# Kernel optimization log

Measured on AMD Instinct MI355X. Metric: run time of the kernel, lower is better.

## Reference

```python
import jax, jax.numpy as jnp
import numpy as np

B, N = 8, 48
NEMBED, EMBED_DIM, HID_DIM = 1000, 32, 32
IN_DIM = EMBED_DIM + 1  # feature dim after concatenating xfeat
N_OPS = 8  # exchangeable 3-tensor basis: identity + means over each nonempty axis subset


def setup_inputs() -> dict:
    key = jax.random.key(0)
    k1, k2, k3, k4, k5 = jax.random.split(key, 5)
    xcat = jax.random.randint(k1, (B, N), 0, NEMBED)
    xfeat = jax.random.normal(k2, (B, N), dtype=jnp.float32)
    embed_table = jax.random.normal(k3, (NEMBED, EMBED_DIM), dtype=jnp.float32)
    # SetEq3to3 coefficients: (in_dim, n_basis_ops, out_dim), Glorot-ish scale
    coefs = jax.random.normal(k4, (IN_DIM, N_OPS, HID_DIM), dtype=jnp.float32) * np.sqrt(2.0 / (IN_DIM + HID_DIM))
    eq_bias = jnp.zeros((HID_DIM,), dtype=jnp.float32)
    out_w = jax.random.normal(k5, (HID_DIM, 1), dtype=jnp.float32) * np.sqrt(1.0 / HID_DIM)
    out_b = jnp.zeros((1,), dtype=jnp.float32)
    return {"xcat": xcat, "xfeat": xfeat, "embed_table": embed_table,
            "coefs": coefs, "eq_bias": eq_bias, "out_w": out_w, "out_b": out_b}


def _set_eq3to3(t, coefs, eq_bias):
    # t: (B, d, n, n, n); coefs: (d, 8, h). Each basis op is a mean over a
    # subset of the three set axes (kept as size-1 dims so broadcasting restores shape).
    def mix(op, s):
        return jnp.einsum('bd...,dh->bh...', op, coefs[:, s, :])
    m_i = t.mean(axis=2, keepdims=True)
    m_j = t.mean(axis=3, keepdims=True)
    m_k = t.mean(axis=4, keepdims=True)
    m_ij = m_i.mean(axis=3, keepdims=True)
    m_ik = m_i.mean(axis=4, keepdims=True)
    m_jk = m_j.mean(axis=4, keepdims=True)
    m_ijk = m_ij.mean(axis=4, keepdims=True)
    out = (mix(t, 0) + mix(m_i, 1) + mix(m_j, 2) + mix(m_k, 3)
           + mix(m_ij, 4) + mix(m_ik, 5) + mix(m_jk, 6) + mix(m_ijk, 7))
    return out + eq_bias.reshape(1, -1, 1, 1, 1)  # (B, h, n, n, n)


def reference(xcat, xfeat, embed_table, coefs, eq_bias, out_w, out_b):
    e = embed_table[xcat]                                   # (B, n, d_e)
    x = jnp.concatenate([e, xfeat[..., None]], axis=-1)      # (B, n, d) with d = d_e + 1
    t = jnp.einsum('bid,bjd,bkd->bdijk', x, x, x)            # (B, d, n, n, n)
    y = _set_eq3to3(t, coefs, eq_bias)                       # (B, h, n, n, n)
    y = jnp.transpose(y, (0, 2, 3, 4, 1))                    # (B, n, n, n, h)
    y = jax.nn.relu(y)
    y = y.mean(axis=(1, 2, 3))                               # (B, h) mean pool
    y = jax.nn.relu(y)
    # dropout is inactive in eval mode (training=False)
    return y @ out_w + out_b                                 # (B, 1)
```

## Files before the change

### kernel.cpp

```cpp
#include <hip/hip_runtime.h>
#include <cstdint>
#include <cstddef>

#define BB 8
#define NN 48
#define DD 33
#define XS 40
#define KP 128
#define HH 32
#define MM (NN*NN)
#define NC (NN*HH)
#define TILE 96
#define TM (MM/TILE)
#define TN (NC/TILE)
#define SPLITM 4
#define MQ (TM/SPLITM)
#define NBLK (TN*SPLITM*BB)
#define LDK 136

typedef __attribute__((ext_vector_type(8))) _Float16 f16x8;
typedef __attribute__((ext_vector_type(4))) float f32x4;

__global__ void k_setup(const int* __restrict__ xcat, const float* __restrict__ xfeat,
                        const float* __restrict__ embed, const float* __restrict__ coefs,
                        float* __restrict__ xw, float* __restrict__ sw,
                        float* __restrict__ ct, float* __restrict__ hacc_g,
                        unsigned int* __restrict__ counter) {
    int b = blockIdx.x, t = threadIdx.x;
    if (b < BB) {
        for (int idx = t; idx < NN * XS; idx += 256) {
            int i = idx / XS, d = idx - i * XS;
            float v = 0.f;
            if (d < 32)       v = embed[xcat[b * NN + i] * 32 + d];
            else if (d == 32) v = xfeat[b * NN + i];
            xw[b * NN * XS + idx] = v;
        }
        __syncthreads();
        if (t < XS) {
            float a = 0.f;
            for (int i = 0; i < NN; ++i) a += xw[b * NN * XS + i * XS + t];
            sw[b * XS + t] = a * (1.0f / 48.0f);
        }
    } else if (b == BB) {
        for (int idx = t; idx < 8 * HH * XS; idx += 256) {
            int qh = idx / XS, d = idx - qh * XS;
            int q = qh >> 5, h = qh & 31;
            ct[idx] = (d < DD) ? coefs[(d * 8 + q) * HH + h] : 0.f;
        }
    } else {
        if (t < BB * HH) hacc_g[t] = 0.f;
        if (t == 0) *counter = 0u;
    }
}

__global__ __launch_bounds__(256, 2) void k_gemm(
        const float* __restrict__ xw, const float* __restrict__ sw,
        const float* __restrict__ ct, const float* __restrict__ eq_bias,
        float* __restrict__ hacc_g, unsigned int* __restrict__ counter,
        const float* __restrict__ out_w, const float* __restrict__ out_b,
        float* __restrict__ out) {
    __shared__ __align__(16) _Float16 As[TILE][LDK];
    __shared__ __align__(16) _Float16 Bs[TILE][LDK];
    __shared__ float gbuf[TILE];
    __shared__ float hacc[HH];
    __shared__ int lastFlag;

    int t = threadIdx.x;
    int bx = blockIdx.x, my = blockIdx.y, b = blockIdx.z;
    int N0 = bx * TILE;
    const float* xb = xw + b * NN * XS;
    const float* sb = sw + b * XS;

    if (t < HH) hacc[t] = 0.f;
    if (t < TILE) {
        int n = N0 + t, k = n >> 5, h = n & 31;
        const float* xk = xb + k * XS;
        const float* c4 = ct + (4 * HH + h) * XS;
        const float* c7 = ct + (7 * HH + h) * XS;
        float g = 0.f;
        for (int d = 0; d < DD; ++d) {
            float sd = sb[d];
            g += sd * sd * (c4[d] * xk[d] + c7[d] * sd);
        }
        gbuf[t] = g + eq_bias[h];
    }
    __syncthreads();

    for (int c = 0; c < 6; ++c) {
        int ch = c * 256 + t;
        int row = ch >> 4, d0 = (ch & 15) * 8;
        int n = N0 + row, k = n >> 5, h = n & 31;
        const float* xk = xb + k * XS;
        f16x8 v;
        if (d0 < 120) {
            int seg = (d0 >= 80) ? 2 : (d0 >= 40) ? 1 : 0;
            int d = d0 - seg * 40;
            const int QA[3] = {0, 2, 1}, QB[3] = {3, 6, 5};
            const float* ca = ct + (QA[seg] * HH + h) * XS + d;
            const float* cb = ct + (QB[seg] * HH + h) * XS + d;
            f32x4 ca0 = *(const f32x4*)(ca),     ca1 = *(const f32x4*)(ca + 4);
            f32x4 cb0 = *(const f32x4*)(cb),     cb1 = *(const f32x4*)(cb + 4);
            f32x4 xk0 = *(const f32x4*)(xk + d), xk1 = *(const f32x4*)(xk + d + 4);
            f32x4 sb0 = *(const f32x4*)(sb + d), sb1 = *(const f32x4*)(sb + d + 4);
            f32x4 r0 = ca0 * xk0 + cb0 * sb0;
            f32x4 r1 = ca1 * xk1 + cb1 * sb1;
            for (int e = 0; e < 4; ++e) { v[e] = (_Float16)r0[e]; v[4 + e] = (_Float16)r1[e]; }
        } else {
            v = (f16x8){0, 0, 0, 0, 0, 0, 0, 0};
            v[0] = (_Float16)gbuf[row];
        }
        *(f16x8*)&Bs[row][d0] = v;
    }

    auto buildA = [&](int mt) {
        int M0 = (my * MQ + mt) * TILE;
        for (int c = 0; c < 6; ++c) {
            int ch = c * 256 + t;
            int row = ch >> 4, d0 = (ch & 15) * 8;
            int grow = M0 + row;
            int i = grow / NN, j = grow - i * NN;
            f16x8 v;
            if (d0 < 120) {
                int seg = (d0 >= 80) ? 2 : (d0 >= 40) ? 1 : 0;
                int d = d0 - seg * 40;
                const float* p1 = (seg == 2) ? (xb + j * XS) : (xb + i * XS);
                const float* p2 = (seg == 0) ? (xb + j * XS) : sb;
                f32x4 a0 = *(const f32x4*)(p1 + d), a1 = *(const f32x4*)(p1 + d + 4);
                f32x4 b0 = *(const f32x4*)(p2 + d), b1 = *(const f32x4*)(p2 + d + 4);
                f32x4 r0 = a0 * b0, r1 = a1 * b1;
                for (int e = 0; e < 4; ++e) { v[e] = (_Float16)r0[e]; v[4 + e] = (_Float16)r1[e]; }
            } else {
                v = (f16x8){0, 0, 0, 0, 0, 0, 0, 0};
                v[0] = (_Float16)1.f;
            }
            *(f16x8*)&As[row][d0] = v;
        }
    };

    buildA(0);
    __syncthreads();

    int lane = t & 63, wave = t >> 6;
    int wm = (wave >> 1) * 48, wn = (wave & 1) * 48;
    int lrow = lane & 15, quad = lane >> 4;

    f16x8 bf[3][4];
#pragma unroll
    for (int nt = 0; nt < 3; ++nt)
#pragma unroll
        for (int ks = 0; ks < 4; ++ks)
            bf[nt][ks] = *(const f16x8*)&Bs[wn + nt * 16 + lrow][ks * 32 + quad * 8];

    float fs[3] = {0.f, 0.f, 0.f};
    for (int mt = 0; mt < MQ; ++mt) {
        f32x4 acc[3][3];
#pragma unroll
        for (int m3 = 0; m3 < 3; ++m3)
#pragma unroll
            for (int nt = 0; nt < 3; ++nt)
                acc[m3][nt] = (f32x4){0.f, 0.f, 0.f, 0.f};

#pragma unroll
        for (int ks = 0; ks < 4; ++ks) {
            f16x8 af[3];
#pragma unroll
            for (int m3 = 0; m3 < 3; ++m3)
                af[m3] = *(const f16x8*)&As[wm + m3 * 16 + lrow][ks * 32 + quad * 8];
#pragma unroll
            for (int m3 = 0; m3 < 3; ++m3)
#pragma unroll
                for (int nt = 0; nt < 3; ++nt)
                    acc[m3][nt] = __builtin_amdgcn_mfma_f32_16x16x32_f16(af[m3], bf[nt][ks], acc[m3][nt], 0, 0, 0);
        }

#pragma unroll
        for (int m3 = 0; m3 < 3; ++m3)
#pragma unroll
            for (int nt = 0; nt < 3; ++nt)
#pragma unroll
                for (int r = 0; r < 4; ++r)
                    fs[nt] += fmaxf(acc[m3][nt][r], 0.f);

        __syncthreads();
        if (mt + 1 < MQ) {
            buildA(mt + 1);
            __syncthreads();
        }
    }

#pragma unroll
    for (int nt = 0; nt < 3; ++nt) {
        float v = fs[nt];
        v += __shfl_xor(v, 16);
        v += __shfl_xor(v, 32);
        if (lane < 16) atomicAdd(&hacc[(wn + nt * 16 + lane) & 31], v);
    }
    __syncthreads();
    if (t < HH) atomicAdd(&hacc_g[b * HH + t], hacc[t]);
    __threadfence();
    __syncthreads();
    if (t == 0) {
        unsigned int tk = atomicAdd(counter, 1u);
        lastFlag = (tk == NBLK - 1) ? 1 : 0;
    }
    __syncthreads();

    if (lastFlag) {
        int bb = t >> 5, h2 = t & 31;
        float v = atomicAdd(&hacc_g[bb * HH + h2], 0.f);
        float m = v * (1.0f / 110592.0f);
        float r = fmaxf(m, 0.f) * out_w[h2];
        r += __shfl_xor(r, 1);
        r += __shfl_xor(r, 2);
        r += __shfl_xor(r, 4);
        r += __shfl_xor(r, 8);
        r += __shfl_xor(r, 16);
        if (h2 == 0) out[bb] = r + out_b[0];
    }
}

extern "C" void kernel_launch(void* const* d_in, const int* in_sizes, int n_in,
                              void* d_out, int out_size, void* d_ws, size_t ws_size,
                              hipStream_t stream) {
    (void)in_sizes; (void)n_in; (void)out_size; (void)ws_size;
    const int*   xcat    = (const int*)d_in[0];
    const float* xfeat   = (const float*)d_in[1];
    const float* embed   = (const float*)d_in[2];
    const float* coefs   = (const float*)d_in[3];
    const float* eq_bias = (const float*)d_in[4];
    const float* out_w   = (const float*)d_in[5];
    const float* out_b   = (const float*)d_in[6];
    float* out = (float*)d_out;

    char* w = (char*)d_ws;
    float*        xw      = (float*)(w + 0);
    float*        sw      = (float*)(w + 61440);
    float*        ct      = (float*)(w + 62720);
    float*        hacc_g  = (float*)(w + 103680);
    unsigned int* counter = (unsigned int*)(w + 104704);

    k_setup<<<dim3(BB + 2), dim3(256), 0, stream>>>(xcat, xfeat, embed, coefs,
                                                    xw, sw, ct, hacc_g, counter);
    k_gemm<<<dim3(TN, SPLITM, BB), dim3(256), 0, stream>>>(xw, sw, ct, eq_bias,
                                                           hacc_g, counter,
                                                           out_w, out_b, out);
}
```

Baseline: 126.4 us.

## Give each GEMM block a single M tile instead of looping over tiles

Removes the per-block loop over M tiles (SPLITM=4, 6 tiles each) so that each block computes one 96x96 output tile. The grid grows from 16x4x8 to 16x24x8 blocks, and occupancy is raised to 3 blocks per CU. This adds parallelism and removes the serialized build/sync loop. In exchange, every block rebuilds its B tile and gbuf, and the number of global atomic adds and counter increments goes up sixfold.

```diff
diff --git a/kernel.cpp b/kernel.cpp
--- a/kernel.cpp
+++ b/kernel.cpp
@@ -13,9 +13,7 @@
 #define TILE 96
 #define TM (MM/TILE)
 #define TN (NC/TILE)
-#define SPLITM 4
-#define MQ (TM/SPLITM)
-#define NBLK (TN*SPLITM*BB)
+#define NBLK (TM*TN*BB)
 #define LDK 136
 
 typedef __attribute__((ext_vector_type(8))) _Float16 f16x8;
@@ -53,7 +51,7 @@
     }
 }
 
-__global__ __launch_bounds__(256, 2) void k_gemm(
+__global__ __launch_bounds__(256, 3) void k_gemm(
         const float* __restrict__ xw, const float* __restrict__ sw,
         const float* __restrict__ ct, const float* __restrict__ eq_bias,
         float* __restrict__ hacc_g, unsigned int* __restrict__ counter,
@@ -66,8 +64,8 @@
     __shared__ int lastFlag;
 
     int t = threadIdx.x;
-    int bx = blockIdx.x, my = blockIdx.y, b = blockIdx.z;
-    int N0 = bx * TILE;
+    int bx = blockIdx.x, by = blockIdx.y, b = blockIdx.z;
+    int N0 = bx * TILE, M0 = by * TILE;
     const float* xb = xw + b * NN * XS;
     const float* sb = sw + b * XS;
 
@@ -89,34 +87,30 @@
     for (int c = 0; c < 6; ++c) {
         int ch = c * 256 + t;
         int row = ch >> 4, d0 = (ch & 15) * 8;
-        int n = N0 + row, k = n >> 5, h = n & 31;
-        const float* xk = xb + k * XS;
-        f16x8 v;
-        if (d0 < 120) {
-            int seg = (d0 >= 80) ? 2 : (d0 >= 40) ? 1 : 0;
-            int d = d0 - seg * 40;
-            const int QA[3] = {0, 2, 1}, QB[3] = {3, 6, 5};
-            const float* ca = ct + (QA[seg] * HH + h) * XS + d;
-            const float* cb = ct + (QB[seg] * HH + h) * XS + d;
-            f32x4 ca0 = *(const f32x4*)(ca),     ca1 = *(const f32x4*)(ca + 4);
-            f32x4 cb0 = *(const f32x4*)(cb),     cb1 = *(const f32x4*)(cb + 4);
-            f32x4 xk0 = *(const f32x4*)(xk + d), xk1 = *(const f32x4*)(xk + d + 4);
-            f32x4 sb0 = *(const f32x4*)(sb + d), sb1 = *(const f32x4*)(sb + d + 4);
-            f32x4 r0 = ca0 * xk0 + cb0 * sb0;
-            f32x4 r1 = ca1 * xk1 + cb1 * sb1;
-            for (int e = 0; e < 4; ++e) { v[e] = (_Float16)r0[e]; v[4 + e] = (_Float16)r1[e]; }
-        } else {
-            v = (f16x8){0, 0, 0, 0, 0, 0, 0, 0};
-            v[0] = (_Float16)gbuf[row];
-        }
-        *(f16x8*)&Bs[row][d0] = v;
-    }
-
-    auto buildA = [&](int mt) {
-        int M0 = (my * MQ + mt) * TILE;
-        for (int c = 0; c < 6; ++c) {
-            int ch = c * 256 + t;
-            int row = ch >> 4, d0 = (ch & 15) * 8;
+        {
+            int n = N0 + row, k = n >> 5, h = n & 31;
+            const float* xk = xb + k * XS;
+            f16x8 v;
+            if (d0 < 120) {
+                int seg = (d0 >= 80) ? 2 : (d0 >= 40) ? 1 : 0;
+                int d = d0 - seg * 40;
+                const int QA[3] = {0, 2, 1}, QB[3] = {3, 6, 5};
+                const float* ca = ct + (QA[seg] * HH + h) * XS + d;
+                const float* cb = ct + (QB[seg] * HH + h) * XS + d;
+                f32x4 ca0 = *(const f32x4*)(ca),     ca1 = *(const f32x4*)(ca + 4);
+                f32x4 cb0 = *(const f32x4*)(cb),     cb1 = *(const f32x4*)(cb + 4);
+                f32x4 xk0 = *(const f32x4*)(xk + d), xk1 = *(const f32x4*)(xk + d + 4);
+                f32x4 sb0 = *(const f32x4*)(sb + d), sb1 = *(const f32x4*)(sb + d + 4);
+                f32x4 r0 = ca0 * xk0 + cb0 * sb0;
+                f32x4 r1 = ca1 * xk1 + cb1 * sb1;
+                for (int e = 0; e < 4; ++e) { v[e] = (_Float16)r0[e]; v[4 + e] = (_Float16)r1[e]; }
+            } else {
+                v = (f16x8){0, 0, 0, 0, 0, 0, 0, 0};
+                v[0] = (_Float16)gbuf[row];
+            }
+            *(f16x8*)&Bs[row][d0] = v;
+        }
+        {
             int grow = M0 + row;
             int i = grow / NN, j = grow - i * NN;
             f16x8 v;
@@ -135,58 +129,44 @@
             }
             *(f16x8*)&As[row][d0] = v;
         }
-    };
-
-    buildA(0);
+    }
     __syncthreads();
 
     int lane = t & 63, wave = t >> 6;
     int wm = (wave >> 1) * 48, wn = (wave & 1) * 48;
     int lrow = lane & 15, quad = lane >> 4;
 
-    f16x8 bf[3][4];
-#pragma unroll
-    for (int nt = 0; nt < 3; ++nt)
-#pragma unroll
-        for (int ks = 0; ks < 4; ++ks)
-            bf[nt][ks] = *(const f16x8*)&Bs[wn + nt * 16 + lrow][ks * 32 + quad * 8];
+    f32x4 acc[3][3];
+#pragma unroll
+    for (int m3 = 0; m3 < 3; ++m3)
+#pragma unroll
+        for (int nt = 0; nt < 3; ++nt)
+            acc[m3][nt] = (f32x4){0.f, 0.f, 0.f, 0.f};
+
+#pragma unroll
+    for (int ks = 0; ks < 4; ++ks) {
+        f16x8 af[3], bf[3];
+#pragma unroll
+        for (int m3 = 0; m3 < 3; ++m3)
+            af[m3] = *(const f16x8*)&As[wm + m3 * 16 + lrow][ks * 32 + quad * 8];
+#pragma unroll
+        for (int nt = 0; nt < 3; ++nt)
+            bf[nt] = *(const f16x8*)&Bs[wn + nt * 16 + lrow][ks * 32 + quad * 8];
+#pragma unroll
+        for (int m3 = 0; m3 < 3; ++m3)
+#pragma unroll
+            for (int nt = 0; nt < 3; ++nt)
+                acc[m3][nt] = __builtin_amdgcn_mfma_f32_16x16x32_f16(af[m3], bf[nt], acc[m3][nt], 0, 0, 0);
+    }
 
     float fs[3] = {0.f, 0.f, 0.f};
-    for (int mt = 0; mt < MQ; ++mt) {
-        f32x4 acc[3][3];
-#pragma unroll
-        for (int m3 = 0; m3 < 3; ++m3)
-#pragma unroll
-            for (int nt = 0; nt < 3; ++nt)
-                acc[m3][nt] = (f32x4){0.f, 0.f, 0.f, 0.f};
-
-#pragma unroll
-        for (int ks = 0; ks < 4; ++ks) {
-            f16x8 af[3];
-#pragma unroll
-            for (int m3 = 0; m3 < 3; ++m3)
-                af[m3] = *(const f16x8*)&As[wm + m3 * 16 + lrow][ks * 32 + quad * 8];
-#pragma unroll
-            for (int m3 = 0; m3 < 3; ++m3)
-#pragma unroll
-                for (int nt = 0; nt < 3; ++nt)
-                    acc[m3][nt] = __builtin_amdgcn_mfma_f32_16x16x32_f16(af[m3], bf[nt][ks], acc[m3][nt], 0, 0, 0);
-        }
-
-#pragma unroll
-        for (int m3 = 0; m3 < 3; ++m3)
-#pragma unroll
-            for (int nt = 0; nt < 3; ++nt)
-#pragma unroll
-                for (int r = 0; r < 4; ++r)
-                    fs[nt] += fmaxf(acc[m3][nt][r], 0.f);
-
-        __syncthreads();
-        if (mt + 1 < MQ) {
-            buildA(mt + 1);
-            __syncthreads();
-        }
-    }
+#pragma unroll
+    for (int m3 = 0; m3 < 3; ++m3)
+#pragma unroll
+        for (int nt = 0; nt < 3; ++nt)
+#pragma unroll
+            for (int r = 0; r < 4; ++r)
+                fs[nt] += fmaxf(acc[m3][nt][r], 0.f);
 
 #pragma unroll
     for (int nt = 0; nt < 3; ++nt) {
@@ -241,7 +221,7 @@
 
     k_setup<<<dim3(BB + 2), dim3(256), 0, stream>>>(xcat, xfeat, embed, coefs,
                                                     xw, sw, ct, hacc_g, counter);
-    k_gemm<<<dim3(TN, SPLITM, BB), dim3(256), 0, stream>>>(xw, sw, ct, eq_bias,
-                                                           hacc_g, counter,
-                                                           out_w, out_b, out);
+    k_gemm<<<dim3(TN, TM, BB), dim3(256), 0, stream>>>(xw, sw, ct, eq_bias,
+                                                       hacc_g, counter,
+                                                       out_w, out_b, out);
 }
```

Result: slower. 294.4 us (+132.9%).
